# Optimization experiments

Measured on AMD Instinct MI355X. Metric: run time of the kernel, lower is better.

## Reference

```python
import jax, jax.numpy as jnp
import numpy as np

B, N, K, DIM = 2, 20000, 16, 256


def _mlp(x, W, b):
    # torch nn.Linear: x @ W.T + b, then LeakyReLU(0.1)
    return jax.nn.leaky_relu(x @ W.T + b, negative_slope=0.1)


def _lfa(features, geom, idx, W, b):
    # features: [B, N, C]; geom: [B, N, K, 4]; idx: [B, N, K]
    t = _mlp(geom, W, b)                                  # [B, N, K, d_lfa]
    fn = jax.vmap(lambda f, i: f[i])(features, idx)       # gather neighbors: [B, N, K, C]
    # mean over K of concat == concat of means (faithful, avoids big concat)
    return jnp.concatenate([t.mean(axis=2), fn.mean(axis=2)], axis=-1)


def _linear_init(key, out_f, in_f):
    k1, k2 = jax.random.split(key)
    bound = 1.0 / np.sqrt(in_f)
    W = jax.random.uniform(k1, (out_f, in_f), jnp.float32, -bound, bound)
    b = jax.random.uniform(k2, (out_f,), jnp.float32, -bound, bound)
    return W, b


def setup_inputs() -> dict:
    key = jax.random.key(0)
    ks = jax.random.split(key, 8)
    W_init, b_init = _linear_init(ks[0], DIM // 4, DIM)
    W_l1, b_l1 = _linear_init(ks[1], DIM // 4, 4)
    W_l2, b_l2 = _linear_init(ks[2], DIM // 2, 4)
    W_fin, b_fin = _linear_init(ks[3], DIM, DIM)
    W_id, b_id = _linear_init(ks[4], DIM, DIM)
    return {
        "input_tensor": jax.random.normal(ks[5], (B, N, DIM), jnp.float32),
        "geometric_features": jax.random.normal(ks[6], (B, N, K, 4), jnp.float32),
        "neighbor_indices": jax.random.randint(ks[7], (B, N, K), 0, N, jnp.int64 if jax.config.jax_enable_x64 else jnp.int32),
        "W_init": W_init, "b_init": b_init,
        "W_l1": W_l1, "b_l1": b_l1,
        "W_l2": W_l2, "b_l2": b_l2,
        "W_fin": W_fin, "b_fin": b_fin,
        "W_id": W_id, "b_id": b_id,
    }


def reference(input_tensor, geometric_features, neighbor_indices,
              W_init, b_init, W_l1, b_l1, W_l2, b_l2,
              W_fin, b_fin, W_id, b_id):
    residual = input_tensor
    x = _mlp(input_tensor, W_init, b_init)                       # [B, N, dim/4]
    x = _lfa(x, geometric_features, neighbor_indices, W_l1, b_l1)  # [B, N, dim/2]
    x = _lfa(x, geometric_features, neighbor_indices, W_l2, b_l2)  # [B, N, dim]
    x = _mlp(x, W_fin, b_fin)
    return x + _mlp(residual, W_id, b_id)
```

## Files before the change

### kernel.cpp

```cpp
#include <hip/hip_runtime.h>
#include <hip/hip_bf16.h>

#define BN   40000
#define NPTS 20000
#define KNN  16
#define DIM  256

typedef __attribute__((ext_vector_type(8))) short bf16x8;
typedef __attribute__((ext_vector_type(4))) float f32x4;
typedef __attribute__((ext_vector_type(16))) float f32x16;

__device__ __forceinline__ float lrelu(float v) { return fmaxf(v, 0.1f * v); }
__device__ __forceinline__ float bs2f(short s) {
    union { unsigned u; float f; } c; c.u = ((unsigned)(unsigned short)s) << 16;
    return c.f;
}
__device__ __forceinline__ short f2bs(float f) {
    __hip_bfloat16 h = __float2bfloat16(f);
    return *reinterpret_cast<short*>(&h);
}
__device__ __forceinline__ bf16x8 ldf32_bf16x8(const float* p) {
    const float4 a = ((const float4*)p)[0];
    const float4 b = ((const float4*)p)[1];
    bf16x8 r;
    r[0]=f2bs(a.x); r[1]=f2bs(a.y); r[2]=f2bs(a.z); r[3]=f2bs(a.w);
    r[4]=f2bs(b.x); r[5]=f2bs(b.y); r[6]=f2bs(b.z); r[7]=f2bs(b.w);
    return r;
}

__device__ __forceinline__ void dma16(const void* g, void* l) {
    __builtin_amdgcn_global_load_lds(
        (const __attribute__((address_space(1))) unsigned int*)g,
        (__attribute__((address_space(3))) unsigned int*)l, 16, 0, 0);
}

__global__ void __launch_bounds__(256) geom_kernel(
    const float* __restrict__ geom,
    const float* __restrict__ W1, const float* __restrict__ B1,
    const float* __restrict__ W2, const float* __restrict__ B2,
    const int* __restrict__ idxw, int* __restrict__ flag,
    const float* __restrict__ Wf, const float* __restrict__ Wi,
    const float* __restrict__ Wn,
    short* __restrict__ Wt, short* __restrict__ Wnt,
    __hip_bfloat16* __restrict__ x2,
    __hip_bfloat16* __restrict__ x3)
{
    if (blockIdx.x >= 5001) {
        int t = (blockIdx.x - 5001) * 256 + threadIdx.x;
        if (t < 32768) {
            int mat = (t >> 14) & 1;
            int tt  = t & 16383;
            float4 v = mat ? ((const float4*)Wi)[tt] : ((const float4*)Wf)[tt];
            int n  = tt >> 6;
            int k  = (tt & 63) * 4;
            int kk = k >> 5, q = (k >> 3) & 3, j = k & 7;
            short4 o; o.x=f2bs(v.x); o.y=f2bs(v.y); o.z=f2bs(v.z); o.w=f2bs(v.w);
            *(short4*)(Wt + ((size_t)((kk*2 + mat)*4 + q))*2048 + n*8 + j) = o;
        } else {
            int tt = t - 32768;
            float4 v = ((const float4*)Wn)[tt];
            int n  = tt >> 6;
            int k  = (tt & 63) * 4;
            int kk = k >> 5, q = (k >> 3) & 3, j = k & 7;
            short4 o; o.x=f2bs(v.x); o.y=f2bs(v.y); o.z=f2bs(v.z); o.w=f2bs(v.w);
            *(short4*)(Wnt + ((size_t)((kk*4 + q)*64 + n))*8 + j) = o;
        }
        return;
    }
    if (blockIdx.x == 5000) {
        __shared__ int red[256];
        int t = threadIdx.x;
        int v = 0;
#pragma unroll
        for (int it = 0; it < 64; ++it)
            v |= idxw[2 * (t + it * 256) + 1];
        red[t] = v;
        __syncthreads();
        for (int s = 128; s > 0; s >>= 1) {
            if (t < s) red[t] |= red[t + s];
            __syncthreads();
        }
        if (t == 0) *flag = (red[0] != 0) ? 1 : 0;
        return;
    }
    const int lane = threadIdx.x & 63;
    const int wv   = threadIdx.x >> 6;
    const int p0   = (blockIdx.x * 4 + wv) * 2;
    const int c31  = lane & 31;
    const int hi   = lane >> 5;

    bf16x8 a = (bf16x8){0,0,0,0,0,0,0,0};
    if (hi == 0) {
        const float4 g = *(const float4*)(
            geom + ((size_t)(p0 + (c31 >> 4)) * KNN + (c31 & 15)) * 4);
        a[0]=f2bs(g.x); a[1]=f2bs(g.y); a[2]=f2bs(g.z); a[3]=f2bs(g.w);
    }
    bf16x8 bfr[6]; float bv[6];
#pragma unroll
    for (int tt = 0; tt < 6; ++tt) {
        bfr[tt] = (bf16x8){0,0,0,0,0,0,0,0};
        const float* Wrow;
        if (tt < 2) { Wrow = W1 + (size_t)(tt*32 + c31) * 4;     bv[tt] = B1[tt*32 + c31]; }
        else        { Wrow = W2 + (size_t)((tt-2)*32 + c31) * 4; bv[tt] = B2[(tt-2)*32 + c31]; }
        if (hi == 0) {
            const float4 w4 = *(const float4*)Wrow;
            bfr[tt][0]=f2bs(w4.x); bfr[tt][1]=f2bs(w4.y);
            bfr[tt][2]=f2bs(w4.z); bfr[tt][3]=f2bs(w4.w);
        }
    }
    f32x16 acc[6];
#pragma unroll
    for (int tt = 0; tt < 6; ++tt) {
#pragma unroll
        for (int i = 0; i < 16; ++i) acc[tt][i] = 0.f;
        acc[tt] = __builtin_amdgcn_mfma_f32_32x32x16_bf16(a, bfr[tt], acc[tt], 0, 0, 0);
    }
#pragma unroll
    for (int tt = 0; tt < 6; ++tt) {
        float sA = 0.f, sB = 0.f;
#pragma unroll
        for (int i = 0; i < 8; ++i)  sA += lrelu(acc[tt][i]     + bv[tt]);
#pragma unroll
        for (int i = 0; i < 8; ++i)  sB += lrelu(acc[tt][i + 8] + bv[tt]);
        sA += __shfl_xor(sA, 32, 64);
        sB += __shfl_xor(sB, 32, 64);
        const float s = (hi ? sB : sA) * (1.f / 16.f);
        const short v = f2bs(s);
        if (tt < 2) ((short*)x2)[(size_t)(p0 + hi) * 128 + tt*32 + c31] = v;
        else        ((short*)x3)[(size_t)(p0 + hi) * 256 + (tt-2)*32 + c31] = v;
    }
}

__global__ void __launch_bounds__(256) mlp_init_mfma(
    const float* __restrict__ X,
    const short* __restrict__ Wnt,
    const float* __restrict__ bias,
    __hip_bfloat16* __restrict__ Y)
{
    __shared__ short wbuf[16384];
    int t = threadIdx.x;
    int wave = t >> 6, lane = t & 63;
    int r = lane & 15, q = lane >> 4;
    {
        const char* W8 = (const char*)Wnt;
        char* L8 = (char*)wbuf;
#pragma unroll
        for (int rd = 0; rd < 8; ++rd) {
            int off = (wave * 8 + rd) * 1024 + lane * 16;
            dma16(W8 + off, L8 + off);
        }
    }
    int m0 = blockIdx.x * 64 + wave * 16;
    const float* Xs = X + (size_t)(m0 + r) * DIM + q * 8;
    bf16x8 a[8];
#pragma unroll
    for (int kk = 0; kk < 8; ++kk) a[kk] = ldf32_bf16x8(Xs + kk * 32);
    __syncthreads();

    f32x4 acc[4];
#pragma unroll
    for (int nt = 0; nt < 4; ++nt) acc[nt] = (f32x4){0.f,0.f,0.f,0.f};
#pragma unroll
    for (int kk = 0; kk < 8; ++kk) {
#pragma unroll
        for (int nt = 0; nt < 4; ++nt) {
            bf16x8 b = *(const bf16x8*)&wbuf[((kk*4 + q)*64 + nt*16 + r) * 8];
            acc[nt] = __builtin_amdgcn_mfma_f32_16x16x32_bf16(a[kk], b, acc[nt], 0, 0, 0);
        }
    }
#pragma unroll
    for (int nt = 0; nt < 4; ++nt) {
        int col = nt * 16 + r;
        float bvx = bias[col];
#pragma unroll
        for (int i = 0; i < 4; ++i) {
            float v = lrelu(acc[nt][i] + bvx);
            Y[(size_t)(m0 + q*4 + i) * 64 + col] = __float2bfloat16(v);
        }
    }
}

__global__ void __launch_bounds__(256) gather1_kernel(
    const int* __restrict__ idxw, const int* __restrict__ flag,
    const __hip_bfloat16* __restrict__ x1,
    __hip_bfloat16* __restrict__ x2)
{
    int t = blockIdx.x * 256 + threadIdx.x;
    int p = t >> 3, j = t & 7;
    int lane = threadIdx.x & 63;
    int dual = (*flag == 0) ? 2 : 1;
    int base = (p >= NPTS) ? NPTS : 0;
    int i0 = idxw[((size_t)p * 16 + 2*j)     * dual];
    int i1 = idxw[((size_t)p * 16 + 2*j + 1) * dual];
    int g8 = lane & 56;
    float acc[8];
#pragma unroll
    for (int i = 0; i < 8; ++i) acc[i] = 0.f;
#pragma unroll
    for (int k = 0; k < 8; ++k) {
        int rA = base + __shfl(i0, g8 + k, 64);
        int rB = base + __shfl(i1, g8 + k, 64);
        bf16x8 vA = *(const bf16x8*)((const short*)x1 + (size_t)rA * 64 + j * 8);
        bf16x8 vB = *(const bf16x8*)((const short*)x1 + (size_t)rB * 64 + j * 8);
#pragma unroll
        for (int i = 0; i < 8; ++i) acc[i] += bs2f(vA[i]) + bs2f(vB[i]);
    }
    bf16x8 o;
#pragma unroll
    for (int i = 0; i < 8; ++i) o[i] = f2bs(acc[i] * (1.f/16.f));
    *(bf16x8*)((short*)x2 + (size_t)p * 128 + 64 + j * 8) = o;
}

__global__ void __launch_bounds__(256) gather2_kernel(
    const int* __restrict__ idxw, const int* __restrict__ flag,
    const __hip_bfloat16* __restrict__ x2,
    __hip_bfloat16* __restrict__ x3)
{
    int t = blockIdx.x * 256 + threadIdx.x;
    int p = t >> 4, j = t & 15;
    int lane = threadIdx.x & 63;
    int dual = (*flag == 0) ? 2 : 1;
    int base = (p >= NPTS) ? NPTS : 0;
    int myi = idxw[((size_t)p * 16 + j) * dual];
    int g16 = lane & 48;
    float acc[8];
#pragma unroll
    for (int i = 0; i < 8; ++i) acc[i] = 0.f;
#pragma unroll
    for (int k = 0; k < KNN; ++k) {
        int row = base + __shfl(myi, g16 + k, 64);
        bf16x8 v = *(const bf16x8*)((const short*)x2 + (size_t)row * 128 + j * 8);
#pragma unroll
        for (int i = 0; i < 8; ++i) acc[i] += bs2f(v[i]);
    }
    bf16x8 o;
#pragma unroll
    for (int i = 0; i < 8; ++i) o[i] = f2bs(acc[i] * (1.f/16.f));
    *(bf16x8*)((short*)x3 + (size_t)p * 256 + 128 + j * 8) = o;
}

__global__ void __launch_bounds__(512, 2) final_mfma(
    const __hip_bfloat16* __restrict__ X3,
    const float* __restrict__ RES,
    const short* __restrict__ Wt,
    const float* __restrict__ Bf,
    const float* __restrict__ Bi,
    float* __restrict__ OUT)
{
    __shared__ short lw[65536];
    const int t    = threadIdx.x;
    const int wave = t >> 6, lane = t & 63;
    const int r = lane & 15, q = lane >> 4;
    const int rg = wave >> 1, cg = wave & 1;
    const int ch = blockIdx.x & 1;
    const int p0 = (blockIdx.x >> 1) * 320;

    {
        const char* WtB = (const char*)Wt;
        char* L = (char*)lw;
#pragma unroll
        for (int i = 0; i < 16; ++i) {
            int c = wave * 8 + (i >> 1);
            int d = i & 1;
            int mat = c >> 5, kk = (c >> 2) & 7, qq = c & 3;
            int src_sh = ((kk * 2 + mat) * 4 + qq) * 2048 + ch * 1024;
            dma16(WtB + (size_t)src_sh * 2 + d * 1024 + lane * 16,
                  L + (c * 2 + d) * 1024 + lane * 16);
        }
    }
    const int cb = ch * 128 + cg * 64;
    float bfv[4], biv[4];
#pragma unroll
    for (int nt = 0; nt < 4; ++nt) {
        bfv[nt] = Bf[cb + nt * 16 + r];
        biv[nt] = Bi[cb + nt * 16 + r];
    }
    __syncthreads();

    const short* bpf = lw + q * 1024 + (cg * 64 + r) * 8;
    const short* bpi = bpf + 32768;

#pragma unroll
    for (int tt = 0; tt < 5; ++tt) {
        const int row = p0 + tt * 64 + rg * 16 + r;
        const short* x3r = (const short*)X3 + (size_t)row * DIM + q * 8;
        const float* rsr = RES + (size_t)row * DIM + q * 8;

        bf16x8 a1[8];
        float4 rw[16];
#pragma unroll
        for (int kk = 0; kk < 8; ++kk) {
            rw[2*kk]   = ((const float4*)rsr)[kk * 8];
            rw[2*kk+1] = ((const float4*)rsr)[kk * 8 + 1];
            a1[kk] = *(const bf16x8*)(x3r + kk * 32);
        }

        f32x4 acc1[4], acc2[4];
#pragma unroll
        for (int nt = 0; nt < 4; ++nt) {
            acc1[nt] = (f32x4){0.f,0.f,0.f,0.f};
            acc2[nt] = (f32x4){0.f,0.f,0.f,0.f};
        }
#pragma unroll
        for (int kk = 0; kk < 8; ++kk) {
            bf16x8 a2;
            {
                const float4 lo = rw[2*kk], hi = rw[2*kk+1];
                a2[0]=f2bs(lo.x); a2[1]=f2bs(lo.y); a2[2]=f2bs(lo.z); a2[3]=f2bs(lo.w);
                a2[4]=f2bs(hi.x); a2[5]=f2bs(hi.y); a2[6]=f2bs(hi.z); a2[7]=f2bs(hi.w);
            }
#pragma unroll
            for (int nt = 0; nt < 4; ++nt) {
                bf16x8 b1 = *(const bf16x8*)(bpf + kk * 4096 + nt * 128);
                bf16x8 b2 = *(const bf16x8*)(bpi + kk * 4096 + nt * 128);
                acc1[nt] = __builtin_amdgcn_mfma_f32_16x16x32_bf16(a1[kk], b1, acc1[nt], 0, 0, 0);
                acc2[nt] = __builtin_amdgcn_mfma_f32_16x16x32_bf16(a2,    b2, acc2[nt], 0, 0, 0);
            }
        }
#pragma unroll
        for (int nt = 0; nt < 4; ++nt) {
            const int col = cb + nt * 16 + r;
#pragma unroll
            for (int i = 0; i < 4; ++i) {
                float v = lrelu(acc1[nt][i] + bfv[nt]) + lrelu(acc2[nt][i] + biv[nt]);
                OUT[(size_t)(p0 + tt * 64 + rg * 16 + q * 4 + i) * DIM + col] = v;
            }
        }
    }
}

extern "C" void kernel_launch(void* const* d_in, const int* in_sizes, int n_in,
                              void* d_out, int out_size, void* d_ws, size_t ws_size,
                              hipStream_t stream)
{
    const float* input  = (const float*)d_in[0];
    const float* geom   = (const float*)d_in[1];
    const int*   idxw   = (const int*)d_in[2];
    const float* W_init = (const float*)d_in[3];
    const float* b_init = (const float*)d_in[4];
    const float* W_l1   = (const float*)d_in[5];
    const float* b_l1   = (const float*)d_in[6];
    const float* W_l2   = (const float*)d_in[7];
    const float* b_l2   = (const float*)d_in[8];
    const float* W_fin  = (const float*)d_in[9];
    const float* b_fin  = (const float*)d_in[10];
    const float* W_id   = (const float*)d_in[11];
    const float* b_id   = (const float*)d_in[12];
    float* out = (float*)d_out;

    char* ws = (char*)d_ws;
    int* flag = (int*)ws;
    short* Wt  = (short*)(ws + 16);
    short* Wnt = (short*)(ws + 16 + 262144);
    __hip_bfloat16* x2 = (__hip_bfloat16*)(ws + 16 + 5120000);
    __hip_bfloat16* x3 = (__hip_bfloat16*)(ws + 16 + 15360000);
    __hip_bfloat16* x1 = (__hip_bfloat16*)d_out;

    geom_kernel<<<5145, 256, 0, stream>>>(geom, W_l1, b_l1, W_l2, b_l2,
                                          idxw, flag, W_fin, W_id, W_init,
                                          Wt, Wnt, x2, x3);
    mlp_init_mfma<<<625, 256, 0, stream>>>(input, Wnt, b_init, x1);
    gather1_kernel<<<1250, 256, 0, stream>>>(idxw, flag, x1, x2);
    gather2_kernel<<<2500, 256, 0, stream>>>(idxw, flag, x2, x3);
    final_mfma<<<250, 512, 0, stream>>>(x3, input, Wt, b_fin, b_id, out);
}
```

Measured before the change: 206.4 us.

## Persist geom waves over multiple points and restructure final GEMM tiling

geom_kernel now has each wave process 8 point-pairs in a loop, prefetching the next geometry slice and loading the weight fragments once, so far fewer blocks are launched. final_mfma now has each block cover 128 rows and all 256 output columns. It loads the activation and residual fragments once and reuses them for both column halves, streaming the second half of the weights into LDS after the first half is consumed. A live1 guard handles the partial last block. The aim is to stop reading X3 and RES twice across the column-split blocks and to amortize weight setup, at the cost of higher register pressure and fewer blocks for parallelism.

New measurement: 212.0 us. 1.03x slower.

```diff
diff --git a/kernel.cpp b/kernel.cpp
--- a/kernel.cpp
+++ b/kernel.cpp
@@ -45,8 +45,8 @@
     __hip_bfloat16* __restrict__ x2,
     __hip_bfloat16* __restrict__ x3)
 {
-    if (blockIdx.x >= 5001) {
-        int t = (blockIdx.x - 5001) * 256 + threadIdx.x;
+    if (blockIdx.x >= 626) {
+        int t = (blockIdx.x - 626) * 256 + threadIdx.x;
         if (t < 32768) {
             int mat = (t >> 14) & 1;
             int tt  = t & 16383;
@@ -67,7 +67,7 @@
         }
         return;
     }
-    if (blockIdx.x == 5000) {
+    if (blockIdx.x == 625) {
         __shared__ int red[256];
         int t = threadIdx.x;
         int v = 0;
@@ -85,16 +85,10 @@
     }
     const int lane = threadIdx.x & 63;
     const int wv   = threadIdx.x >> 6;
-    const int p0   = (blockIdx.x * 4 + wv) * 2;
     const int c31  = lane & 31;
     const int hi   = lane >> 5;
-
-    bf16x8 a = (bf16x8){0,0,0,0,0,0,0,0};
-    if (hi == 0) {
-        const float4 g = *(const float4*)(
-            geom + ((size_t)(p0 + (c31 >> 4)) * KNN + (c31 & 15)) * 4);
-        a[0]=f2bs(g.x); a[1]=f2bs(g.y); a[2]=f2bs(g.z); a[3]=f2bs(g.w);
-    }
+    const int wglob = blockIdx.x * 4 + wv;
+
     bf16x8 bfr[6]; float bv[6];
 #pragma unroll
     for (int tt = 0; tt < 6; ++tt) {
@@ -108,26 +102,45 @@
             bfr[tt][2]=f2bs(w4.z); bfr[tt][3]=f2bs(w4.w);
         }
     }
-    f32x16 acc[6];
-#pragma unroll
-    for (int tt = 0; tt < 6; ++tt) {
-#pragma unroll
-        for (int i = 0; i < 16; ++i) acc[tt][i] = 0.f;
-        acc[tt] = __builtin_amdgcn_mfma_f32_32x32x16_bf16(a, bfr[tt], acc[tt], 0, 0, 0);
-    }
-#pragma unroll
-    for (int tt = 0; tt < 6; ++tt) {
-        float sA = 0.f, sB = 0.f;
-#pragma unroll
-        for (int i = 0; i < 8; ++i)  sA += lrelu(acc[tt][i]     + bv[tt]);
-#pragma unroll
-        for (int i = 0; i < 8; ++i)  sB += lrelu(acc[tt][i + 8] + bv[tt]);
-        sA += __shfl_xor(sA, 32, 64);
-        sB += __shfl_xor(sB, 32, 64);
-        const float s = (hi ? sB : sA) * (1.f / 16.f);
-        const short v = f2bs(s);
-        if (tt < 2) ((short*)x2)[(size_t)(p0 + hi) * 128 + tt*32 + c31] = v;
-        else        ((short*)x3)[(size_t)(p0 + hi) * 256 + (tt-2)*32 + c31] = v;
+    f32x16 ZR;
+#pragma unroll
+    for (int i = 0; i < 16; ++i) ZR[i] = 0.f;
+
+    float4 g = (float4){0.f,0.f,0.f,0.f};
+    if (hi == 0)
+        g = *(const float4*)(geom +
+            ((size_t)((wglob * 8) * 2 + (c31 >> 4)) * KNN + (c31 & 15)) * 4);
+
+#pragma unroll
+    for (int it = 0; it < 8; ++it) {
+        const int p0 = (wglob * 8 + it) * 2;
+        const float4 gc = g;
+        if (it < 7 && hi == 0)
+            g = *(const float4*)(geom +
+                ((size_t)(p0 + 2 + (c31 >> 4)) * KNN + (c31 & 15)) * 4);
+
+        bf16x8 a = (bf16x8){0,0,0,0,0,0,0,0};
+        if (hi == 0) { a[0]=f2bs(gc.x); a[1]=f2bs(gc.y); a[2]=f2bs(gc.z); a[3]=f2bs(gc.w); }
+
+        f32x16 acc[6];
+#pragma unroll
+        for (int tt = 0; tt < 6; ++tt)
+            acc[tt] = __builtin_amdgcn_mfma_f32_32x32x16_bf16(a, bfr[tt], ZR, 0, 0, 0);
+
+#pragma unroll
+        for (int tt = 0; tt < 6; ++tt) {
+            float sA = 0.f, sB = 0.f;
+#pragma unroll
+            for (int i = 0; i < 8; ++i)  sA += lrelu(acc[tt][i]     + bv[tt]);
+#pragma unroll
+            for (int i = 0; i < 8; ++i)  sB += lrelu(acc[tt][i + 8] + bv[tt]);
+            sA += __shfl_xor(sA, 32, 64);
+            sB += __shfl_xor(sB, 32, 64);
+            const float s = (hi ? sB : sA) * (1.f / 16.f);
+            const short v = f2bs(s);
+            if (tt < 2) ((short*)x2)[(size_t)(p0 + hi) * 128 + tt*32 + c31] = v;
+            else        ((short*)x3)[(size_t)(p0 + hi) * 256 + (tt-2)*32 + c31] = v;
+        }
     }
 }
 
@@ -252,78 +265,100 @@
     const int wave = t >> 6, lane = t & 63;
     const int r = lane & 15, q = lane >> 4;
     const int rg = wave >> 1, cg = wave & 1;
-    const int ch = blockIdx.x & 1;
-    const int p0 = (blockIdx.x >> 1) * 320;
-
-    {
-        const char* WtB = (const char*)Wt;
-        char* L = (char*)lw;
-#pragma unroll
-        for (int i = 0; i < 16; ++i) {
-            int c = wave * 8 + (i >> 1);
-            int d = i & 1;
-            int mat = c >> 5, kk = (c >> 2) & 7, qq = c & 3;
-            int src_sh = ((kk * 2 + mat) * 4 + qq) * 2048 + ch * 1024;
-            dma16(WtB + (size_t)src_sh * 2 + d * 1024 + lane * 16,
-                  L + (c * 2 + d) * 1024 + lane * 16);
-        }
-    }
-    const int cb = ch * 128 + cg * 64;
-    float bfv[4], biv[4];
-#pragma unroll
-    for (int nt = 0; nt < 4; ++nt) {
-        bfv[nt] = Bf[cb + nt * 16 + r];
-        biv[nt] = Bi[cb + nt * 16 + r];
-    }
-    __syncthreads();
-
-    const short* bpf = lw + q * 1024 + (cg * 64 + r) * 8;
-    const short* bpi = bpf + 32768;
-
-#pragma unroll
-    for (int tt = 0; tt < 5; ++tt) {
-        const int row = p0 + tt * 64 + rg * 16 + r;
-        const short* x3r = (const short*)X3 + (size_t)row * DIM + q * 8;
-        const float* rsr = RES + (size_t)row * DIM + q * 8;
-
-        bf16x8 a1[8];
-        float4 rw[16];
+    const int p0 = blockIdx.x * 128;
+    const bool live1 = (p0 + 128) <= BN;
+
+    const char* WtB = (const char*)Wt;
+    char* L = (char*)lw;
+#pragma unroll
+    for (int i = 0; i < 16; ++i) {
+        int c = wave * 8 + (i >> 1);
+        int d = i & 1;
+        int mat = c >> 5, kk = (c >> 2) & 7, qq = c & 3;
+        int src_sh = ((kk * 2 + mat) * 4 + qq) * 2048;
+        dma16(WtB + (size_t)src_sh * 2 + d * 1024 + lane * 16,
+              L + (c * 2 + d) * 1024 + lane * 16);
+    }
+
+    bf16x8 a1[2][8], a2[2][8];
+#pragma unroll
+    for (int rt = 0; rt < 2; ++rt) {
+        if (rt == 1 && !live1) {
+#pragma unroll
+            for (int kk = 0; kk < 8; ++kk) {
+                a1[1][kk] = (bf16x8){0,0,0,0,0,0,0,0};
+                a2[1][kk] = (bf16x8){0,0,0,0,0,0,0,0};
+            }
+        } else {
+            const int row = p0 + rt * 64 + rg * 16 + r;
+            const short* x3r = (const short*)X3 + (size_t)row * DIM + q * 8;
+            const float* rsr = RES + (size_t)row * DIM + q * 8;
+#pragma unroll
+            for (int kk = 0; kk < 8; ++kk) {
+                a1[rt][kk] = *(const bf16x8*)(x3r + kk * 32);
+                a2[rt][kk] = ldf32_bf16x8(rsr + kk * 32);
+            }
+        }
+    }
+
+    const short* bp = lw + q * 1024 + (cg * 64 + r) * 8;
+
+#pragma unroll
+    for (int h = 0; h < 2; ++h) {
+        const int cb = h * 128 + cg * 64;
+        float bfv[4], biv[4];
+#pragma unroll
+        for (int nt = 0; nt < 4; ++nt) {
+            bfv[nt] = Bf[cb + nt * 16 + r];
+            biv[nt] = Bi[cb + nt * 16 + r];
+        }
+        __syncthreads();
+
+        f32x4 acc1[2][4], acc2[2][4];
+#pragma unroll
+        for (int rt = 0; rt < 2; ++rt)
+#pragma unroll
+            for (int nt = 0; nt < 4; ++nt) {
+                acc1[rt][nt] = (f32x4){0.f,0.f,0.f,0.f};
+                acc2[rt][nt] = (f32x4){0.f,0.f,0.f,0.f};
+            }
 #pragma unroll
         for (int kk = 0; kk < 8; ++kk) {
-            rw[2*kk]   = ((const float4*)rsr)[kk * 8];
-            rw[2*kk+1] = ((const float4*)rsr)[kk * 8 + 1];
-            a1[kk] = *(const bf16x8*)(x3r + kk * 32);
-        }
-
-        f32x4 acc1[4], acc2[4];
-#pragma unroll
-        for (int nt = 0; nt < 4; ++nt) {
-            acc1[nt] = (f32x4){0.f,0.f,0.f,0.f};
-            acc2[nt] = (f32x4){0.f,0.f,0.f,0.f};
-        }
-#pragma unroll
-        for (int kk = 0; kk < 8; ++kk) {
-            bf16x8 a2;
-            {
-                const float4 lo = rw[2*kk], hi = rw[2*kk+1];
-                a2[0]=f2bs(lo.x); a2[1]=f2bs(lo.y); a2[2]=f2bs(lo.z); a2[3]=f2bs(lo.w);
-                a2[4]=f2bs(hi.x); a2[5]=f2bs(hi.y); a2[6]=f2bs(hi.z); a2[7]=f2bs(hi.w);
-            }
 #pragma unroll
             for (int nt = 0; nt < 4; ++nt) {
-                bf16x8 b1 = *(const bf16x8*)(bpf + kk * 4096 + nt * 128);
-                bf16x8 b2 = *(const bf16x8*)(bpi + kk * 4096 + nt * 128);
-                acc1[nt] = __builtin_amdgcn_mfma_f32_16x16x32_bf16(a1[kk], b1, acc1[nt], 0, 0, 0);
-                acc2[nt] = __builtin_amdgcn_mfma_f32_16x16x32_bf16(a2,    b2, acc2[nt], 0, 0, 0);
-            }
-        }
-#pragma unroll
-        for (int nt = 0; nt < 4; ++nt) {
-            const int col = cb + nt * 16 + r;
-#pragma unroll
-            for (int i = 0; i < 4; ++i) {
-                float v = lrelu(acc1[nt][i] + bfv[nt]) + lrelu(acc2[nt][i] + biv[nt]);
-                OUT[(size_t)(p0 + tt * 64 + rg * 16 + q * 4 + i) * DIM + col] = v;
+                bf16x8 b1 = *(const bf16x8*)(bp + kk * 4096 + nt * 128);
+                bf16x8 b2 = *(const bf16x8*)(bp + 32768 + kk * 4096 + nt * 128);
+                acc1[0][nt] = __builtin_amdgcn_mfma_f32_16x16x32_bf16(a1[0][kk], b1, acc1[0][nt], 0, 0, 0);
+                acc2[0][nt] = __builtin_amdgcn_mfma_f32_16x16x32_bf16(a2[0][kk], b2, acc2[0][nt], 0, 0, 0);
+                acc1[1][nt] = __builtin_amdgcn_mfma_f32_16x16x32_bf16(a1[1][kk], b1, acc1[1][nt], 0, 0, 0);
+                acc2[1][nt] = __builtin_amdgcn_mfma_f32_16x16x32_bf16(a2[1][kk], b2, acc2[1][nt], 0, 0, 0);
+            }
+        }
+        if (h == 0) {
+            __syncthreads();
+#pragma unroll
+            for (int i = 0; i < 16; ++i) {
+                int c = wave * 8 + (i >> 1);
+                int d = i & 1;
+                int mat = c >> 5, kk2 = (c >> 2) & 7, qq = c & 3;
+                int src_sh = ((kk2 * 2 + mat) * 4 + qq) * 2048 + 1024;
+                dma16(WtB + (size_t)src_sh * 2 + d * 1024 + lane * 16,
+                      L + (c * 2 + d) * 1024 + lane * 16);
+            }
+        }
+#pragma unroll
+        for (int rt = 0; rt < 2; ++rt) {
+            if (rt == 0 || live1) {
+#pragma unroll
+                for (int nt = 0; nt < 4; ++nt) {
+                    const int col = cb + nt * 16 + r;
+#pragma unroll
+                    for (int i = 0; i < 4; ++i) {
+                        float v = lrelu(acc1[rt][nt][i] + bfv[nt])
+                                + lrelu(acc2[rt][nt][i] + biv[nt]);
+                        OUT[(size_t)(p0 + rt*64 + rg*16 + q*4 + i) * DIM + col] = v;
+                    }
+                }
             }
         }
     }
@@ -356,11 +391,11 @@
     __hip_bfloat16* x3 = (__hip_bfloat16*)(ws + 16 + 15360000);
     __hip_bfloat16* x1 = (__hip_bfloat16*)d_out;
 
-    geom_kernel<<<5145, 256, 0, stream>>>(geom, W_l1, b_l1, W_l2, b_l2,
-                                          idxw, flag, W_fin, W_id, W_init,
-                                          Wt, Wnt, x2, x3);
+    geom_kernel<<<770, 256, 0, stream>>>(geom, W_l1, b_l1, W_l2, b_l2,
+                                         idxw, flag, W_fin, W_id, W_init,
+                                         Wt, Wnt, x2, x3);
     mlp_init_mfma<<<625, 256, 0, stream>>>(input, Wnt, b_init, x1);
     gather1_kernel<<<1250, 256, 0, stream>>>(idxw, flag, x1, x2);
     gather2_kernel<<<2500, 256, 0, stream>>>(idxw, flag, x2, x3);
-    final_mfma<<<250, 512, 0, stream>>>(x3, input, Wt, b_fin, b_id, out);
-}
+    final_mfma<<<313, 512, 0, stream>>>(x3, input, Wt, b_fin, b_id, out);
+}
```

## Merge geometry MLP with init MLP and loop geometry points per wave

Applied to the files above, without the earlier changes.

Weight repacking and the index-width flag check move into a small separate prep kernel. The geometry MLP and the init MLP now run as one launch: the first 625 blocks do the geometry work and the rest do the init GEMM. Each geometry wave now handles 8 point pairs instead of one, prefetching the next geometry row while MFMAs run, and the bias/zero setup is amortised across those iterations. The risk is that geometry blocks also reserve the 32KB shared weight buffer, which can lower occupancy, and the loop carries a serial dependency.

After: 195.8 us. 1.05x faster.

```diff
diff --git a/kernel.cpp b/kernel.cpp
--- a/kernel.cpp
+++ b/kernel.cpp
@@ -34,40 +34,13 @@
         (__attribute__((address_space(3))) unsigned int*)l, 16, 0, 0);
 }
 
-__global__ void __launch_bounds__(256) geom_kernel(
-    const float* __restrict__ geom,
-    const float* __restrict__ W1, const float* __restrict__ B1,
-    const float* __restrict__ W2, const float* __restrict__ B2,
+__global__ void __launch_bounds__(256) prep_kernel(
     const int* __restrict__ idxw, int* __restrict__ flag,
     const float* __restrict__ Wf, const float* __restrict__ Wi,
     const float* __restrict__ Wn,
-    short* __restrict__ Wt, short* __restrict__ Wnt,
-    __hip_bfloat16* __restrict__ x2,
-    __hip_bfloat16* __restrict__ x3)
-{
-    if (blockIdx.x >= 5001) {
-        int t = (blockIdx.x - 5001) * 256 + threadIdx.x;
-        if (t < 32768) {
-            int mat = (t >> 14) & 1;
-            int tt  = t & 16383;
-            float4 v = mat ? ((const float4*)Wi)[tt] : ((const float4*)Wf)[tt];
-            int n  = tt >> 6;
-            int k  = (tt & 63) * 4;
-            int kk = k >> 5, q = (k >> 3) & 3, j = k & 7;
-            short4 o; o.x=f2bs(v.x); o.y=f2bs(v.y); o.z=f2bs(v.z); o.w=f2bs(v.w);
-            *(short4*)(Wt + ((size_t)((kk*2 + mat)*4 + q))*2048 + n*8 + j) = o;
-        } else {
-            int tt = t - 32768;
-            float4 v = ((const float4*)Wn)[tt];
-            int n  = tt >> 6;
-            int k  = (tt & 63) * 4;
-            int kk = k >> 5, q = (k >> 3) & 3, j = k & 7;
-            short4 o; o.x=f2bs(v.x); o.y=f2bs(v.y); o.z=f2bs(v.z); o.w=f2bs(v.w);
-            *(short4*)(Wnt + ((size_t)((kk*4 + q)*64 + n))*8 + j) = o;
-        }
-        return;
-    }
-    if (blockIdx.x == 5000) {
+    short* __restrict__ Wt, short* __restrict__ Wnt)
+{
+    if (blockIdx.x == 0) {
         __shared__ int red[256];
         int t = threadIdx.x;
         int v = 0;
@@ -83,18 +56,91 @@
         if (t == 0) *flag = (red[0] != 0) ? 1 : 0;
         return;
     }
+    int t = (blockIdx.x - 1) * 256 + threadIdx.x;
+    if (t < 32768) {
+        int mat = (t >> 14) & 1;
+        int tt  = t & 16383;
+        float4 v = mat ? ((const float4*)Wi)[tt] : ((const float4*)Wf)[tt];
+        int n  = tt >> 6;
+        int k  = (tt & 63) * 4;
+        int kk = k >> 5, q = (k >> 3) & 3, j = k & 7;
+        short4 o; o.x=f2bs(v.x); o.y=f2bs(v.y); o.z=f2bs(v.z); o.w=f2bs(v.w);
+        *(short4*)(Wt + ((size_t)((kk*2 + mat)*4 + q))*2048 + n*8 + j) = o;
+    } else {
+        int tt = t - 32768;
+        float4 v = ((const float4*)Wn)[tt];
+        int n  = tt >> 6;
+        int k  = (tt & 63) * 4;
+        int kk = k >> 5, q = (k >> 3) & 3, j = k & 7;
+        short4 o; o.x=f2bs(v.x); o.y=f2bs(v.y); o.z=f2bs(v.z); o.w=f2bs(v.w);
+        *(short4*)(Wnt + ((size_t)((kk*4 + q)*64 + n))*8 + j) = o;
+    }
+}
+
+__global__ void __launch_bounds__(256) stage2_kernel(
+    const float* __restrict__ geom,
+    const float* __restrict__ W1, const float* __restrict__ B1,
+    const float* __restrict__ W2, const float* __restrict__ B2,
+    const float* __restrict__ X,
+    const short* __restrict__ Wnt,
+    const float* __restrict__ b_init,
+    __hip_bfloat16* __restrict__ x2,
+    __hip_bfloat16* __restrict__ x3,
+    __hip_bfloat16* __restrict__ x1)
+{
+    __shared__ short wbuf[16384];
+
+    if (blockIdx.x >= 625) {
+        int bid = blockIdx.x - 625;
+        int t = threadIdx.x;
+        int wave = t >> 6, lane = t & 63;
+        int r = lane & 15, q = lane >> 4;
+        {
+            const char* W8 = (const char*)Wnt;
+            char* L8 = (char*)wbuf;
+#pragma unroll
+            for (int rd = 0; rd < 8; ++rd) {
+                int off = (wave * 8 + rd) * 1024 + lane * 16;
+                dma16(W8 + off, L8 + off);
+            }
+        }
+        int m0 = bid * 64 + wave * 16;
+        const float* Xs = X + (size_t)(m0 + r) * DIM + q * 8;
+        bf16x8 a[8];
+#pragma unroll
+        for (int kk = 0; kk < 8; ++kk) a[kk] = ldf32_bf16x8(Xs + kk * 32);
+        __syncthreads();
+
+        f32x4 acc[4];
+#pragma unroll
+        for (int nt = 0; nt < 4; ++nt) acc[nt] = (f32x4){0.f,0.f,0.f,0.f};
+#pragma unroll
+        for (int kk = 0; kk < 8; ++kk) {
+#pragma unroll
+            for (int nt = 0; nt < 4; ++nt) {
+                bf16x8 b = *(const bf16x8*)&wbuf[((kk*4 + q)*64 + nt*16 + r) * 8];
+                acc[nt] = __builtin_amdgcn_mfma_f32_16x16x32_bf16(a[kk], b, acc[nt], 0, 0, 0);
+            }
+        }
+#pragma unroll
+        for (int nt = 0; nt < 4; ++nt) {
+            int col = nt * 16 + r;
+            float bvx = b_init[col];
+#pragma unroll
+            for (int i = 0; i < 4; ++i) {
+                float v = lrelu(acc[nt][i] + bvx);
+                x1[(size_t)(m0 + q*4 + i) * 64 + col] = __float2bfloat16(v);
+            }
+        }
+        return;
+    }
+
     const int lane = threadIdx.x & 63;
     const int wv   = threadIdx.x >> 6;
-    const int p0   = (blockIdx.x * 4 + wv) * 2;
     const int c31  = lane & 31;
     const int hi   = lane >> 5;
-
-    bf16x8 a = (bf16x8){0,0,0,0,0,0,0,0};
-    if (hi == 0) {
-        const float4 g = *(const float4*)(
-            geom + ((size_t)(p0 + (c31 >> 4)) * KNN + (c31 & 15)) * 4);
-        a[0]=f2bs(g.x); a[1]=f2bs(g.y); a[2]=f2bs(g.z); a[3]=f2bs(g.w);
-    }
+    const int wglob = blockIdx.x * 4 + wv;
+
     bf16x8 bfr[6]; float bv[6];
 #pragma unroll
     for (int tt = 0; tt < 6; ++tt) {
@@ -108,74 +154,44 @@
             bfr[tt][2]=f2bs(w4.z); bfr[tt][3]=f2bs(w4.w);
         }
     }
-    f32x16 acc[6];
-#pragma unroll
-    for (int tt = 0; tt < 6; ++tt) {
-#pragma unroll
-        for (int i = 0; i < 16; ++i) acc[tt][i] = 0.f;
-        acc[tt] = __builtin_amdgcn_mfma_f32_32x32x16_bf16(a, bfr[tt], acc[tt], 0, 0, 0);
-    }
-#pragma unroll
-    for (int tt = 0; tt < 6; ++tt) {
-        float sA = 0.f, sB = 0.f;
-#pragma unroll
-        for (int i = 0; i < 8; ++i)  sA += lrelu(acc[tt][i]     + bv[tt]);
-#pragma unroll
-        for (int i = 0; i < 8; ++i)  sB += lrelu(acc[tt][i + 8] + bv[tt]);
-        sA += __shfl_xor(sA, 32, 64);
-        sB += __shfl_xor(sB, 32, 64);
-        const float s = (hi ? sB : sA) * (1.f / 16.f);
-        const short v = f2bs(s);
-        if (tt < 2) ((short*)x2)[(size_t)(p0 + hi) * 128 + tt*32 + c31] = v;
-        else        ((short*)x3)[(size_t)(p0 + hi) * 256 + (tt-2)*32 + c31] = v;
-    }
-}
-
-__global__ void __launch_bounds__(256) mlp_init_mfma(
-    const float* __restrict__ X,
-    const short* __restrict__ Wnt,
-    const float* __restrict__ bias,
-    __hip_bfloat16* __restrict__ Y)
-{
-    __shared__ short wbuf[16384];
-    int t = threadIdx.x;
-    int wave = t >> 6, lane = t & 63;
-    int r = lane & 15, q = lane >> 4;
-    {
-        const char* W8 = (const char*)Wnt;
-        char* L8 = (char*)wbuf;
-#pragma unroll
-        for (int rd = 0; rd < 8; ++rd) {
-            int off = (wave * 8 + rd) * 1024 + lane * 16;
-            dma16(W8 + off, L8 + off);
-        }
-    }
-    int m0 = blockIdx.x * 64 + wave * 16;
-    const float* Xs = X + (size_t)(m0 + r) * DIM + q * 8;
-    bf16x8 a[8];
-#pragma unroll
-    for (int kk = 0; kk < 8; ++kk) a[kk] = ldf32_bf16x8(Xs + kk * 32);
-    __syncthreads();
-
-    f32x4 acc[4];
-#pragma unroll
-    for (int nt = 0; nt < 4; ++nt) acc[nt] = (f32x4){0.f,0.f,0.f,0.f};
-#pragma unroll
-    for (int kk = 0; kk < 8; ++kk) {
-#pragma unroll
-        for (int nt = 0; nt < 4; ++nt) {
-            bf16x8 b = *(const bf16x8*)&wbuf[((kk*4 + q)*64 + nt*16 + r) * 8];
-            acc[nt] = __builtin_amdgcn_mfma_f32_16x16x32_bf16(a[kk], b, acc[nt], 0, 0, 0);
-        }
-    }
-#pragma unroll
-    for (int nt = 0; nt < 4; ++nt) {
-        int col = nt * 16 + r;
-        float bvx = bias[col];
-#pragma unroll
-        for (int i = 0; i < 4; ++i) {
-            float v = lrelu(acc[nt][i] + bvx);
-            Y[(size_t)(m0 + q*4 + i) * 64 + col] = __float2bfloat16(v);
+    f32x16 ZR;
+#pragma unroll
+    for (int i = 0; i < 16; ++i) ZR[i] = 0.f;
+
+    float4 g = (float4){0.f,0.f,0.f,0.f};
+    if (hi == 0)
+        g = *(const float4*)(geom +
+            ((size_t)((wglob * 8) * 2 + (c31 >> 4)) * KNN + (c31 & 15)) * 4);
+
+#pragma unroll
+    for (int it = 0; it < 8; ++it) {
+        const int p0 = (wglob * 8 + it) * 2;
+        const float4 gc = g;
+        if (it < 7 && hi == 0)
+            g = *(const float4*)(geom +
+                ((size_t)(p0 + 2 + (c31 >> 4)) * KNN + (c31 & 15)) * 4);
+
+        bf16x8 a = (bf16x8){0,0,0,0,0,0,0,0};
+        if (hi == 0) { a[0]=f2bs(gc.x); a[1]=f2bs(gc.y); a[2]=f2bs(gc.z); a[3]=f2bs(gc.w); }
+
+        f32x16 acc[6];
+#pragma unroll
+        for (int tt = 0; tt < 6; ++tt)
+            acc[tt] = __builtin_amdgcn_mfma_f32_32x32x16_bf16(a, bfr[tt], ZR, 0, 0, 0);
+
+#pragma unroll
+        for (int tt = 0; tt < 6; ++tt) {
+            float sA = 0.f, sB = 0.f;
+#pragma unroll
+            for (int i = 0; i < 8; ++i)  sA += lrelu(acc[tt][i]     + bv[tt]);
+#pragma unroll
+            for (int i = 0; i < 8; ++i)  sB += lrelu(acc[tt][i + 8] + bv[tt]);
+            sA += __shfl_xor(sA, 32, 64);
+            sB += __shfl_xor(sB, 32, 64);
+            const float s = (hi ? sB : sA) * (1.f / 16.f);
+            const short v = f2bs(s);
+            if (tt < 2) ((short*)x2)[(size_t)(p0 + hi) * 128 + tt*32 + c31] = v;
+            else        ((short*)x3)[(size_t)(p0 + hi) * 256 + (tt-2)*32 + c31] = v;
         }
     }
 }
@@ -356,10 +372,10 @@
     __hip_bfloat16* x3 = (__hip_bfloat16*)(ws + 16 + 15360000);
     __hip_bfloat16* x1 = (__hip_bfloat16*)d_out;
 
-    geom_kernel<<<5145, 256, 0, stream>>>(geom, W_l1, b_l1, W_l2, b_l2,
-                                          idxw, flag, W_fin, W_id, W_init,
-                                          Wt, Wnt, x2, x3);
-    mlp_init_mfma<<<625, 256, 0, stream>>>(input, Wnt, b_init, x1);
+    prep_kernel<<<145, 256, 0, stream>>>(idxw, flag, W_fin, W_id, W_init,
+                                         Wt, Wnt);
+    stage2_kernel<<<1250, 256, 0, stream>>>(geom, W_l1, b_l1, W_l2, b_l2,
+                                            input, Wnt, b_init, x2, x3, x1);
     gather1_kernel<<<1250, 256, 0, stream>>>(idxw, flag, x1, x2);
     gather2_kernel<<<2500, 256, 0, stream>>>(idxw, flag, x2, x3);
     final_mfma<<<250, 512, 0, stream>>>(x3, input, Wt, b_fin, b_id, out);
```
